# Kernel optimization log

Hardware: AMD Instinct MI355X
Metric: run time of the kernel (lower is better)

## Reference

```python
import math
import jax, jax.numpy as jnp
import numpy as np

D_MODEL = 1024
N_HEADS = 16
HEAD_DIM = 64          # block_size
NUM_RULES = 64
RANK = 8               # proj_rank = round(sqrt(head_dim)); also router_rank
SHARED_RANK = 32       # round(sqrt(d_model))
NUM_BLOCKS = 16        # min(in,out)//block_size = 1024//64; total_block_dim == d_model
B, S = 4, 1024
ROPE_BASE = 10000.0


def setup_inputs() -> dict:
    key = jax.random.key(0)
    ks = iter(jax.random.split(key, 32))
    def nrm(shape, s=0.02):
        return jax.random.normal(next(ks), shape, dtype=jnp.float32) * s
    inp = {
        "x": jax.random.normal(next(ks), (B, S, D_MODEL), dtype=jnp.float32),
        "target_rule_ids": jax.random.randint(next(ks), (B, S), 0, NUM_RULES),
    }
    for p in ("q", "k", "v", "o"):
        inp[p + "_si"] = nrm((D_MODEL, SHARED_RANK))
        inp[p + "_so"] = nrm((SHARED_RANK, D_MODEL))
        inp[p + "_ri"] = nrm((NUM_RULES, HEAD_DIM, RANK))
        inp[p + "_ro"] = nrm((NUM_RULES, RANK, HEAD_DIM))
        inp[p + "_lg"] = nrm((NUM_RULES, NUM_BLOCKS), 1.0 / math.sqrt(NUM_BLOCKS))
    inp["router_q"] = nrm((NUM_RULES, RANK))
    inp["router_k"] = nrm((NUM_RULES, RANK))
    return inp


def _rule_proj(x, rules, si, so, ri, ro, lg):
    """RuleAwareProjection.forward_rules_batched, de-permuted.

    The torch code argsorts tokens by rule, zero-pads per-rule buckets, runs
    bmm per rule and scatters back; mathematically that equals a per-token
    gather of the rule's low-rank adapter, which is what we compute here.
    x: [N, D_MODEL], rules: [N] int.
    """
    base = (x @ si) @ so                                  # shared low-rank path
    xb = x.reshape(-1, NUM_BLOCKS, HEAD_DIM)              # [N, nb, bs]
    h = jnp.einsum('nbs,nsr->nbr', xb, ri[rules])         # [N, nb, rank]
    a = jnp.einsum('nbr,nrt->nbt', h, ro[rules])          # [N, nb, bs]
    # temperature = 1/sqrt(num_blocks) => logits / temperature = logits*sqrt(nb)
    sel = jax.nn.softmax(lg[rules] * math.sqrt(NUM_BLOCKS), axis=-1)
    return base + (a * sel[:, :, None]).reshape(-1, D_MODEL)


def _rope(q, k):
    # q, k: [B, H, S, D]; interleaved-pair rotation, start_pos = 0.
    S_, D = q.shape[2], q.shape[3]
    pos = jnp.arange(S_, dtype=jnp.float32)[:, None]
    div = jnp.exp(jnp.arange(0, D, 2, dtype=jnp.float32) * (-math.log(ROPE_BASE) / D))
    f = pos * div                                         # [S, D/2]
    sin, cos = jnp.sin(f), jnp.cos(f)
    def rot(t):
        t1, t2 = t[..., 0::2], t[..., 1::2]
        return jnp.stack([t1 * cos - t2 * sin, t2 * cos + t1 * sin], axis=-1).reshape(t.shape)
    return rot(q), rot(k)


def reference(x, target_rule_ids,
              q_si, q_so, q_ri, q_ro, q_lg,
              k_si, k_so, k_ri, k_ro, k_lg,
              v_si, v_so, v_ri, v_ro, v_lg,
              o_si, o_so, o_ri, o_ro, o_lg,
              router_q, router_k):
    B_, S_, C = x.shape
    flat_x = x.reshape(-1, C)
    rules = target_rule_ids.reshape(-1)

    q = _rule_proj(flat_x, rules, q_si, q_so, q_ri, q_ro, q_lg)
    k = _rule_proj(flat_x, rules, k_si, k_so, k_ri, k_ro, k_lg)
    v = _rule_proj(flat_x, rules, v_si, v_so, v_ri, v_ro, v_lg)
    q = q.reshape(B_, S_, N_HEADS, HEAD_DIM).transpose(0, 2, 1, 3)
    k = k.reshape(B_, S_, N_HEADS, HEAD_DIM).transpose(0, 2, 1, 3)
    v = v.reshape(B_, S_, N_HEADS, HEAD_DIM).transpose(0, 2, 1, 3)
    q, k = _rope(q, k)

    # rule-routing sparse mask: cosine affinity between token rule embeddings
    rq = router_q[target_rule_ids]                        # [B, S, rank]
    rk = router_k[target_rule_ids]
    rqn = rq / jnp.maximum(jnp.linalg.norm(rq, axis=-1, keepdims=True), 1e-12)
    rkn = rk / jnp.maximum(jnp.linalg.norm(rk, axis=-1, keepdims=True), 1e-12)
    tau = 1.0 / math.log(max(math.e, RANK))
    aff = jnp.einsum('bqr,bkr->bqk', rqn, rkn) / tau       # [B, S, S]
    causal = jnp.tril(jnp.ones((S_, S_), dtype=bool))
    masked = jnp.where(causal[None], aff, -jnp.inf)
    top_k = max(2, int(math.sqrt(S_)))
    if S_ > top_k:
        thr = jax.lax.top_k(masked, top_k)[0][..., -1:]
        rule_mask = (masked >= thr) & causal[None]
    else:
        rule_mask = jnp.broadcast_to(causal[None], masked.shape)

    scores = jnp.einsum('bhqd,bhkd->bhqk', q, k) / math.sqrt(HEAD_DIM)
    scores = jnp.where(rule_mask[:, None], scores, -jnp.inf)
    attn = jax.nn.softmax(scores, axis=-1)
    out = jnp.einsum('bhqk,bhkd->bhqd', attn, v)
    out = out.transpose(0, 2, 1, 3).reshape(-1, C)
    out = _rule_proj(out, rules, o_si, o_so, o_ri, o_ro, o_lg)
    return out.reshape(B_, S_, C)
```

## Files before the change

### kernel.cpp

```cpp
#include <hip/hip_runtime.h>
#include <hip/hip_bf16.h>

#define D_MODEL 1024
#define N_HEADS 16
#define HEAD_DIM 64
#define NUM_RULES 64
#define RANK 8
#define SHARED_RANK 32
#define NUM_BLOCKS_ 16
#define BB 4
#define SS 1024
#define NTOK (BB*SS)
#define NGRP (NTOK/8)
#define NGRP4 (NTOK/4)

typedef __attribute__((ext_vector_type(8))) short bf16x8;
typedef __attribute__((ext_vector_type(4))) float f32x4;

__device__ __forceinline__ float bf2f(unsigned short u) {
  unsigned int i = ((unsigned int)u) << 16;
  float f;
  __builtin_memcpy(&f, &i, 4);
  return f;
}
__device__ __forceinline__ unsigned short f2bf(float f) {
  __hip_bfloat16 h = __float2bfloat16(f);
  unsigned short u;
  __builtin_memcpy(&u, &h, 2);
  return u;
}
__device__ __forceinline__ float u2f(unsigned int i) {
  float f;
  __builtin_memcpy(&f, &i, 4);
  return f;
}
template<bool BF>
__device__ __forceinline__ float ldw(const void* p, size_t i) {
  if (BF) return bf2f(((const unsigned short*)p)[i]);
  else    return ((const float*)p)[i];
}

__device__ __forceinline__ void gload16(const void* g, void* l) {
  __builtin_amdgcn_global_load_lds(
      (const __attribute__((address_space(1))) unsigned int*)g,
      (__attribute__((address_space(3))) unsigned int*)l, 16, 0, 0);
}

__global__ void detect_kernel(const unsigned short* __restrict__ x, int* __restrict__ flag) {
  const int lane = threadIdx.x;
  int good = 0;
  for (int i = 0; i < 4; i++) {
    unsigned short u = x[lane*4 + i];
    int e = (u >> 7) & 0xFF;
    good += (e == 0 || (e >= 100 && e <= 145)) ? 1 : 0;
  }
  for (int off = 32; off; off >>= 1) good += __shfl_xor(good, off);
  if (lane == 0) flag[0] = (good >= 224) ? 1 : 0;
}

template<bool BF>
__device__ __forceinline__ void precompute_body(
    const void* rq, const void* rk,
    const void* qlg, const void* klg, const void* vlg, const void* olg,
    float* __restrict__ M, float* __restrict__ sel)
{
  __shared__ float rqn[64][8], rkn[64][8];
  const int tid = threadIdx.x;
  if (tid < 64) {
    float v[8]; float s = 0.f;
    for (int i = 0; i < 8; i++) { v[i] = ldw<BF>(rq, tid*8+i); s += v[i]*v[i]; }
    float inv = 1.0f / fmaxf(sqrtf(s), 1e-12f);
    for (int i = 0; i < 8; i++) rqn[tid][i] = v[i]*inv;
  } else if (tid < 128) {
    int r = tid - 64;
    float v[8]; float s = 0.f;
    for (int i = 0; i < 8; i++) { v[i] = ldw<BF>(rk, r*8+i); s += v[i]*v[i]; }
    float inv = 1.0f / fmaxf(sqrtf(s), 1e-12f);
    for (int i = 0; i < 8; i++) rkn[r][i] = v[i]*inv;
  }
  __syncthreads();
  const float LN8 = 2.0794415416798357f;
  for (int idx = tid; idx < 64*64; idx += 256) {
    int i = idx >> 6, j = idx & 63;
    float d = 0.f;
    for (int t = 0; t < 8; t++) d += rqn[i][t]*rkn[j][t];
    M[idx] = d * LN8;
  }
  const void* lgs[4] = {qlg, klg, vlg, olg};
  {
    int r = tid & 63;
    const void* lg = lgs[tid >> 6];
    float e[NUM_BLOCKS_]; float mx = -1e30f;
    for (int b = 0; b < NUM_BLOCKS_; b++) {
      e[b] = ldw<BF>(lg, r*NUM_BLOCKS_ + b) * 4.0f;
      mx = fmaxf(mx, e[b]);
    }
    float s = 0.f;
    for (int b = 0; b < NUM_BLOCKS_; b++) { e[b] = expf(e[b]-mx); s += e[b]; }
    float inv = 1.0f/s;
    for (int b = 0; b < NUM_BLOCKS_; b++) sel[tid*NUM_BLOCKS_+b] = e[b]*inv;
  }
}

__global__ void precompute_kernel(
    const void* rq, const void* rk,
    const void* qlg, const void* klg, const void* vlg, const void* olg,
    float* M, float* sel, const int* __restrict__ flag)
{
  if (*flag) precompute_body<true >(rq, rk, qlg, klg, vlg, olg, M, sel);
  else       precompute_body<false>(rq, rk, qlg, klg, vlg, olg, M, sel);
}

__global__ __launch_bounds__(128) void prep_wb_kernel(
    const float* __restrict__ qsi, const float* __restrict__ ksi,
    const float* __restrict__ vsi, const float* __restrict__ osi,
    unsigned short* __restrict__ wh, unsigned short* __restrict__ wl,
    const int* __restrict__ flag)
{
  if (*flag) return;
  const int kt = blockIdx.x, p = blockIdx.y;
  const int tid = threadIdx.x, nt = tid >> 6, lane = tid & 63;
  const float* si = (p==0)?qsi:((p==1)?ksi:((p==2)?vsi:osi));
  const int col = nt*16 + (lane & 15);
  const int k0 = kt*32 + (lane >> 4)*8;
  size_t base = ((((size_t)p*32 + kt)*2 + nt)*64 + lane)*8;
  unsigned short h8[8], l8[8];
  #pragma unroll
  for (int j = 0; j < 8; j++) {
    float f = si[(size_t)(k0 + j)*SHARED_RANK + col];
    unsigned short hu = f2bf(f);
    h8[j] = hu;
    l8[j] = f2bf(f - bf2f(hu));
  }
  #pragma unroll
  for (int j = 0; j < 8; j++) { wh[base + j] = h8[j]; wl[base + j] = l8[j]; }
}

template<int NPROJ>
__device__ __forceinline__ void tt_mfma_body(
    const float* __restrict__ xin,
    const unsigned short* __restrict__ wh, const unsigned short* __restrict__ wl,
    int p0, float* __restrict__ ttg)
{
  const int NT = NPROJ*2;
  const int tile = blockIdx.x;
  const int tid = threadIdx.x, lane = tid & 63, w = tid >> 6;
  const int kq = lane >> 4;
  __shared__ float red[4][64][25];

  f32x4 acc[NT];
  #pragma unroll
  for (int i = 0; i < NT; i++) acc[i] = (f32x4){0.f,0.f,0.f,0.f};

  const float* xrow = xin + (size_t)(tile*16 + (lane & 15))*D_MODEL + kq*8;
  #pragma unroll 2
  for (int s = 0; s < 8; s++) {
    const int kt = w*8 + s;
    float4 a0 = *(const float4*)(xrow + kt*32);
    float4 a1 = *(const float4*)(xrow + kt*32 + 4);
    float av[8] = {a0.x,a0.y,a0.z,a0.w,a1.x,a1.y,a1.z,a1.w};
    bf16x8 ah, al;
    #pragma unroll
    for (int j = 0; j < 8; j++) {
      unsigned short hu = f2bf(av[j]);
      ah[j] = (short)hu;
      al[j] = (short)f2bf(av[j] - bf2f(hu));
    }
    #pragma unroll
    for (int p = 0; p < NPROJ; p++) {
      #pragma unroll
      for (int nt = 0; nt < 2; nt++) {
        size_t bidx = ((((size_t)(p0+p)*32 + kt)*2 + nt)*64 + lane)*8;
        bf16x8 bh = *(const bf16x8*)(wh + bidx);
        bf16x8 bl = *(const bf16x8*)(wl + bidx);
        f32x4 c = acc[p*2+nt];
        c = __builtin_amdgcn_mfma_f32_16x16x32_bf16(ah, bh, c, 0, 0, 0);
        c = __builtin_amdgcn_mfma_f32_16x16x32_bf16(al, bh, c, 0, 0, 0);
        c = __builtin_amdgcn_mfma_f32_16x16x32_bf16(ah, bl, c, 0, 0, 0);
        acc[p*2+nt] = c;
      }
    }
  }
  #pragma unroll
  for (int i = 0; i < NT; i++) {
    red[w][lane][i*4+0] = acc[i][0]; red[w][lane][i*4+1] = acc[i][1];
    red[w][lane][i*4+2] = acc[i][2]; red[w][lane][i*4+3] = acc[i][3];
  }
  __syncthreads();
  if (w == 0) {
    const int tok0 = tile*16 + (lane >> 4)*4;
    #pragma unroll
    for (int i = 0; i < NT; i++) {
      const int ys = i >> 1, jj = (i & 1)*16 + (lane & 15);
      #pragma unroll
      for (int r = 0; r < 4; r++) {
        float sum = red[0][lane][i*4+r] + red[1][lane][i*4+r]
                  + red[2][lane][i*4+r] + red[3][lane][i*4+r];
        ttg[((size_t)ys*NTOK + tok0 + r)*32 + jj] = sum;
      }
    }
  }
}

__global__ __launch_bounds__(256) void A_tt_mfma3(
    const float* __restrict__ xin,
    const unsigned short* __restrict__ wh, const unsigned short* __restrict__ wl,
    float* __restrict__ ttg, const int* __restrict__ flag)
{
  if (*flag) return;
  tt_mfma_body<3>(xin, wh, wl, 0, ttg);
}

__global__ __launch_bounds__(256) void A_tt_mfma1(
    const float* __restrict__ xin,
    const unsigned short* __restrict__ wh, const unsigned short* __restrict__ wl,
    float* __restrict__ ttg, const int* __restrict__ flag)
{
  if (*flag) return;
  tt_mfma_body<1>(xin, wh, wl, 3, ttg);
}

template<int NP>
__device__ __forceinline__ void hh_body(
    const float* __restrict__ xin, const int* __restrict__ rules,
    const float* __restrict__ ri0, const float* __restrict__ ri1,
    const float* __restrict__ ri2, float* __restrict__ hhg)
{
  const int g = blockIdx.x, n0 = g*8, tid = threadIdx.x;
  const int t = tid >> 5, blk = (tid >> 1) & 15, r0 = (tid & 1)*4;
  const int n = n0 + t;
  const int rule = rules[n];
  const float* xb = xin + (size_t)n*D_MODEL + blk*64;
  const float* wb[3];
  wb[0] = ri0 + (size_t)rule*512 + r0;
  if (NP > 1) {
    wb[1] = ri1 + (size_t)rule*512 + r0;
    wb[2] = ri2 + (size_t)rule*512 + r0;
  }
  float a[NP][4];
  #pragma unroll
  for (int p = 0; p < NP; p++) { a[p][0]=0.f; a[p][1]=0.f; a[p][2]=0.f; a[p][3]=0.f; }
  #pragma unroll 4
  for (int k4 = 0; k4 < 16; k4++) {
    float4 xv = *(const float4*)(xb + k4*4);
    #pragma unroll
    for (int q = 0; q < 4; q++) {
      const int k = k4*4 + q;
      float xq = (q==0)?xv.x:((q==1)?xv.y:((q==2)?xv.z:xv.w));
      #pragma unroll
      for (int p = 0; p < NP; p++) {
        float4 wv = *(const float4*)(wb[p] + (size_t)k*8);
        a[p][0] += xq*wv.x; a[p][1] += xq*wv.y; a[p][2] += xq*wv.z; a[p][3] += xq*wv.w;
      }
    }
  }
  #pragma unroll
  for (int p = 0; p < NP; p++) {
    float4 hv; hv.x=a[p][0]; hv.y=a[p][1]; hv.z=a[p][2]; hv.w=a[p][3];
    *(float4*)&hhg[((size_t)p*NTOK + n)*128 + blk*8 + r0] = hv;
  }
}

__global__ __launch_bounds__(256) void A_hh3_f32(
    const float* __restrict__ xin, const int* __restrict__ rules,
    const float* __restrict__ qri, const float* __restrict__ kri,
    const float* __restrict__ vri, float* __restrict__ hhg,
    const int* __restrict__ flag)
{
  if (*flag) return;
  hh_body<3>(xin, rules, qri, kri, vri, hhg);
}

__global__ __launch_bounds__(256) void A_hh1_f32(
    const float* __restrict__ xin, const int* __restrict__ rules,
    const float* __restrict__ ori, float* __restrict__ hhg,
    const int* __restrict__ flag)
{
  if (*flag) return;
  hh_body<1>(xin, rules, ori, ori, ori, hhg);
}

template<bool IN_BF, bool W_BF>
__device__ __forceinline__ void stageA_body(
    const void* __restrict__ xin, const int* __restrict__ rules,
    const void* __restrict__ si, const void* __restrict__ ri,
    float* __restrict__ ttg, float* __restrict__ hhg, int yslot)
{
  const int g = blockIdx.x, n0 = g*8, tid = threadIdx.x;
  __shared__ float xs[8][D_MODEL];
  __shared__ float tpart[8][32][9];
  __shared__ int rl[8];

  #pragma unroll
  for (int t = 0; t < 8; t++) {
    float4 f;
    if (IN_BF) {
      ushort4 u = ((const ushort4*)((const unsigned short*)xin + (size_t)(n0+t)*D_MODEL))[tid];
      f.x = bf2f(u.x); f.y = bf2f(u.y); f.z = bf2f(u.z); f.w = bf2f(u.w);
    } else {
      f = ((const float4*)xin)[(size_t)(n0+t)*(D_MODEL/4) + tid];
    }
    *(float4*)&xs[t][tid*4] = f;
  }
  if (tid < 8) rl[tid] = rules[n0 + tid];
  __syncthreads();

  {
    const int c = tid >> 5, j = tid & 31;
    float p[8];
    #pragma unroll
    for (int t = 0; t < 8; t++) p[t] = 0.f;
    #pragma unroll 4
    for (int d4 = 0; d4 < 32; d4++) {
      const int d = c*128 + d4*4;
      float w0 = ldw<W_BF>(si, (size_t)(d+0)*SHARED_RANK + j);
      float w1 = ldw<W_BF>(si, (size_t)(d+1)*SHARED_RANK + j);
      float w2 = ldw<W_BF>(si, (size_t)(d+2)*SHARED_RANK + j);
      float w3 = ldw<W_BF>(si, (size_t)(d+3)*SHARED_RANK + j);
      #pragma unroll
      for (int t = 0; t < 8; t++) {
        float4 xv = *(const float4*)&xs[t][d];
        p[t] += xv.x*w0 + xv.y*w1 + xv.z*w2 + xv.w*w3;
      }
    }
    #pragma unroll
    for (int t = 0; t < 8; t++) tpart[c][j][t] = p[t];
  }
  __syncthreads();

  {
    const int t = tid >> 5, j = tid & 31;
    float s = 0.f;
    #pragma unroll
    for (int c = 0; c < 8; c++) s += tpart[c][j][t];
    ttg[((size_t)yslot*NTOK + n0 + t)*32 + j] = s;
  }
  {
    const int t = tid >> 5, blk = (tid >> 1) & 15, r0 = (tid & 1)*4;
    const int rule = rl[t];
    float a0=0.f, a1=0.f, a2=0.f, a3=0.f;
    #pragma unroll 4
    for (int k4 = 0; k4 < 16; k4++) {
      const int kk = ((k4 + blk) & 15) * 4;
      float4 xv = *(const float4*)&xs[t][blk*64 + kk];
      #pragma unroll
      for (int q = 0; q < 4; q++) {
        const int k = kk + q;
        float w0,w1,w2,w3;
        if (W_BF) {
          ushort4 u = *(const ushort4*)((const unsigned short*)ri + (size_t)rule*512 + (size_t)k*8 + r0);
          w0=bf2f(u.x); w1=bf2f(u.y); w2=bf2f(u.z); w3=bf2f(u.w);
        } else {
          float4 u = *(const float4*)((const float*)ri + (size_t)rule*512 + (size_t)k*8 + r0);
          w0=u.x; w1=u.y; w2=u.z; w3=u.w;
        }
        float xq = (q==0)?xv.x:((q==1)?xv.y:((q==2)?xv.z:xv.w));
        a0 += xq*w0; a1 += xq*w1; a2 += xq*w2; a3 += xq*w3;
      }
    }
    float4 hv; hv.x=a0; hv.y=a1; hv.z=a2; hv.w=a3;
    *(float4*)&hhg[((size_t)yslot*NTOK + n0 + t)*128 + blk*8 + r0] = hv;
  }
}

__global__ __launch_bounds__(256) void A_qkv_bf16(
    const void* x, const int* rules,
    const void* qsi, const void* qri, const void* ksi, const void* kri,
    const void* vsi, const void* vri,
    float* ttg, float* hhg, const int* __restrict__ flag)
{
  if (!*flag) return;
  const int y = blockIdx.y;
  const void* si = (y==0)?qsi:((y==1)?ksi:vsi);
  const void* ri = (y==0)?qri:((y==1)?kri:vri);
  stageA_body<true,true>(x, rules, si, ri, ttg, hhg, y);
}

__global__ __launch_bounds__(256) void A_o_bf16(
    const void* ain, const int* rules, const void* osi, const void* ori,
    float* ttg, float* hhg, const int* __restrict__ flag)
{
  if (!*flag) return;
  stageA_body<false,true>(ain, rules, osi, ori, ttg, hhg, 0);
}

template<bool W_BF>
__device__ __forceinline__ void stageB_body(
    const float* __restrict__ ttg, const float* __restrict__ hhg,
    const int* __restrict__ rules,
    const void* __restrict__ so, const void* __restrict__ ro,
    const float* __restrict__ sel, void* __restrict__ out,
    int yslot, int do_rope, int out_bf)
{
  const int blk4 = blockIdx.x;
  const int n0 = blk4*4, tid = threadIdx.x;
  __shared__ float tt_lds[32][5];
  __shared__ float hh_lds[4][132];
  __shared__ int rl[4];

  if (tid < 128) {
    const int j = tid >> 2, t4 = tid & 3;
    tt_lds[j][t4] = ttg[((size_t)yslot*NTOK + n0 + t4)*32 + j];
  } else if (tid < 256 && (tid - 128) < 128) {
    const int i = tid - 128;
    const int t4 = i >> 5, c = (i*4) & 127;
    float4 hv = *(const float4*)&hhg[((size_t)yslot*NTOK + n0 + t4)*128 + c];
    *(float4*)&hh_lds[t4][c] = hv;
  }
  if (tid < 4) rl[tid] = rules[n0 + tid];
  __syncthreads();

  const int ch0 = tid*4;
  float a0[4], a1[4], a2[4], a3[4];
  #pragma unroll
  for (int t = 0; t < 4; t++) { a0[t]=0.f; a1[t]=0.f; a2[t]=0.f; a3[t]=0.f; }

  #pragma unroll 4
  for (int j = 0; j < 32; j++) {
    float w0, w1, w2, w3;
    if (W_BF) {
      ushort4 u = *(const ushort4*)((const unsigned short*)so + (size_t)j*D_MODEL + ch0);
      w0=bf2f(u.x); w1=bf2f(u.y); w2=bf2f(u.z); w3=bf2f(u.w);
    } else {
      float4 u = *(const float4*)((const float*)so + (size_t)j*D_MODEL + ch0);
      w0=u.x; w1=u.y; w2=u.z; w3=u.w;
    }
    #pragma unroll
    for (int t = 0; t < 4; t++) {
      float tv = tt_lds[j][t];
      a0[t] += tv*w0; a1[t] += tv*w1; a2[t] += tv*w2; a3[t] += tv*w3;
    }
  }

  const int blk = ch0 >> 6, tc = ch0 & 63;
  float inv0 = 0.f, inv1 = 0.f;
  if (do_rope) {
    inv0 = expf(-(float)tc     * (9.210340371976184f/64.0f));
    inv1 = expf(-(float)(tc+2) * (9.210340371976184f/64.0f));
  }
  #pragma unroll 2
  for (int t = 0; t < 4; t++) {
    const int rule = rl[t];
    float b0=0.f, b1=0.f, b2=0.f, b3=0.f;
    #pragma unroll
    for (int r = 0; r < 8; r++) {
      float w0,w1,w2,w3;
      if (W_BF) {
        ushort4 u = *(const ushort4*)((const unsigned short*)ro + (size_t)rule*512 + r*64 + tc);
        w0=bf2f(u.x); w1=bf2f(u.y); w2=bf2f(u.z); w3=bf2f(u.w);
      } else {
        float4 u = *(const float4*)((const float*)ro + (size_t)rule*512 + r*64 + tc);
        w0=u.x; w1=u.y; w2=u.z; w3=u.w;
      }
      float hv = hh_lds[t][blk*8 + r];
      b0 += hv*w0; b1 += hv*w1; b2 += hv*w2; b3 += hv*w3;
    }
    float sb = sel[rule*NUM_BLOCKS_ + blk];
    float e0 = a0[t] + b0*sb, o0 = a1[t] + b1*sb;
    float e1 = a2[t] + b2*sb, o1 = a3[t] + b3*sb;
    const int n = n0 + t;
    if (do_rope) {
      float spos = (float)(n & (SS-1));
      float sn0, cs0, sn1, cs1;
      sincosf(spos*inv0, &sn0, &cs0);
      sincosf(spos*inv1, &sn1, &cs1);
      float u0 = e0*cs0 - o0*sn0; o0 = o0*cs0 + e0*sn0; e0 = u0;
      float u1 = e1*cs1 - o1*sn1; o1 = o1*cs1 + e1*sn1; e1 = u1;
    }
    if (out_bf) {
      ushort4 uv; uv.x=f2bf(e0); uv.y=f2bf(o0); uv.z=f2bf(e1); uv.w=f2bf(o1);
      *(ushort4*)((unsigned short*)out + (size_t)n*D_MODEL + ch0) = uv;
    } else {
      float4 fv; fv.x=e0; fv.y=o0; fv.z=e1; fv.w=o1;
      *(float4*)((float*)out + (size_t)n*D_MODEL + ch0) = fv;
    }
  }
}

__global__ __launch_bounds__(256) void B_qkv_bf16(
    const float* ttg, const float* hhg, const int* rules,
    const void* qso, const void* qro, const void* kso, const void* kro,
    const void* vso, const void* vro,
    const float* sel, float* qb, unsigned short* kb, unsigned short* vb,
    const int* __restrict__ flag)
{
  if (!*flag) return;
  const int y = blockIdx.y;
  const void* so = (y==0)?qso:((y==1)?kso:vso);
  const void* ro = (y==0)?qro:((y==1)?kro:vro);
  void* out = (y==0)?(void*)qb:((y==1)?(void*)kb:(void*)vb);
  stageB_body<true>(ttg, hhg, rules, so, ro, sel + y*1024, out, y, (y<2)?1:0, (y>=1)?1:0);
}

__global__ __launch_bounds__(256) void B_qkv_f32(
    const float* ttg, const float* hhg, const int* rules,
    const void* qso, const void* qro, const void* kso, const void* kro,
    const void* vso, const void* vro,
    const float* sel, float* qb, unsigned short* kb, unsigned short* vb,
    const int* __restrict__ flag)
{
  if (*flag) return;
  const int y = blockIdx.y;
  const void* so = (y==0)?qso:((y==1)?kso:vso);
  const void* ro = (y==0)?qro:((y==1)?kro:vro);
  void* out = (y==0)?(void*)qb:((y==1)?(void*)kb:(void*)vb);
  stageB_body<false>(ttg, hhg, rules, so, ro, sel + y*1024, out, y, (y<2)?1:0, (y>=1)?1:0);
}

__global__ __launch_bounds__(256) void B_o_bf16(
    const float* ttg, const float* hhg, const int* rules,
    const void* oso, const void* oro, const float* sel, void* out,
    const int* __restrict__ flag)
{
  if (!*flag) return;
  stageB_body<true>(ttg, hhg, rules, oso, oro, sel, out, 0, 0, 1);
}

__global__ __launch_bounds__(256) void B_o_f32(
    const float* ttg, const float* hhg, const int* rules,
    const void* oso, const void* oro, const float* sel, void* out,
    const int* __restrict__ flag)
{
  if (*flag) return;
  stageB_body<false>(ttg, hhg, rules, oso, oro, sel, out, 0, 0, 0);
}

__global__ __launch_bounds__(64) void mask_kernel(
    const int* __restrict__ rules, const float* __restrict__ M,
    unsigned long long* __restrict__ am)
{
  const int bid = blockIdx.x;
  const int b = bid >> 10, qi = bid & 1023;
  const int lane = threadIdx.x;
  __shared__ int rrow[SS];
  __shared__ float val[64];
  __shared__ int cnth[64];
  for (int i = lane; i < SS/4; i += 64)
    ((int4*)rrow)[i] = ((const int4*)(rules + b*SS))[i];
  cnth[lane] = 0;
  __syncthreads();
  for (int k = lane; k <= qi; k += 64) atomicAdd(&cnth[rrow[k]], 1);
  const int qrule = rrow[qi];
  const float myv = M[qrule*64 + lane];
  val[lane] = myv;
  __syncthreads();
  const int c = cnth[lane];
  int A = 0;
  for (int r = 0; r < 64; r++) {
    int cr = __shfl(c, r);
    A += (val[r] > myv) ? cr : 0;
  }
  unsigned long long allowed = __ballot(A < 32);
  if (lane == 0) am[bid] = allowed;
}

__global__ __launch_bounds__(256) void vtrans_kernel(
    const unsigned short* __restrict__ vb, unsigned short* __restrict__ vt)
{
  const int st = blockIdx.x, h = blockIdx.y, b = blockIdx.z;
  __shared__ unsigned short t[64][72];
  const int tid = threadIdx.x;
  #pragma unroll
  for (int it = 0; it < 2; it++) {
    int i = tid + it*256;
    int r = i >> 3, c8 = (i & 7)*8;
    uint4 v = *(const uint4*)(vb + ((size_t)(b*SS + st*64 + r)*D_MODEL + h*HEAD_DIM + c8));
    t[c8+0][r] = (unsigned short)(v.x & 0xffffu);
    t[c8+1][r] = (unsigned short)(v.x >> 16);
    t[c8+2][r] = (unsigned short)(v.y & 0xffffu);
    t[c8+3][r] = (unsigned short)(v.y >> 16);
    t[c8+4][r] = (unsigned short)(v.z & 0xffffu);
    t[c8+5][r] = (unsigned short)(v.z >> 16);
    t[c8+6][r] = (unsigned short)(v.w & 0xffffu);
    t[c8+7][r] = (unsigned short)(v.w >> 16);
  }
  __syncthreads();
  #pragma unroll
  for (int it = 0; it < 2; it++) {
    int i = tid + it*256;
    int d = i >> 3, c8 = i & 7;
    uint4 o = *(const uint4*)&t[d][c8*8];
    *(uint4*)(vt + ((size_t)(b*N_HEADS + h)*HEAD_DIM + d)*SS + st*64 + c8*8) = o;
  }
}

__global__ __launch_bounds__(256) void attn_mfma_kernel(
    const float* __restrict__ qb,
    const unsigned short* __restrict__ kb,
    const unsigned short* __restrict__ vtb,
    const int* __restrict__ rules,
    const unsigned long long* __restrict__ am,
    float* outb)
{
  const int qx = blockIdx.x, b = blockIdx.y, h = blockIdx.z;
  const int tid = threadIdx.x, lane = tid & 63, w = tid >> 6;
  __shared__ unsigned short Ks[2][64*64];
  __shared__ unsigned short Vs[2][64*64];
  __shared__ unsigned short Pl[4][16*64];
  __shared__ int rl[SS];

  ((int4*)rl)[tid] = ((const int4*)(rules + b*SS))[tid];

  const unsigned short* kbase = kb + (size_t)b*SS*D_MODEL + h*HEAD_DIM;
  const unsigned short* vbase = vtb + (size_t)(b*N_HEADS + h)*HEAD_DIM*SS;

  const int srow0 = tid >> 3;
  const int spos  = tid & 7;
  unsigned short* pw = &Pl[w][0];

  for (int halfq = 0; halfq < 2; halfq++) {
    const int qt = halfq ? (15 - qx) : qx;

    const int qa = qt*64 + w*16 + (lane & 15);
    bf16x8 qfrag[2];
    {
      const float* qrow = qb + (size_t)(b*SS + qa)*D_MODEL + h*HEAD_DIM + (lane>>4)*8;
      #pragma unroll
      for (int kc = 0; kc < 2; kc++) {
        float4 f0 = *(const float4*)(qrow + kc*32);
        float4 f1 = *(const float4*)(qrow + kc*32 + 4);
        bf16x8 qv;
        qv[0] = (short)f2bf(f0.x*0.125f); qv[1] = (short)f2bf(f0.y*0.125f);
        qv[2] = (short)f2bf(f0.z*0.125f); qv[3] = (short)f2bf(f0.w*0.125f);
        qv[4] = (short)f2bf(f1.x*0.125f); qv[5] = (short)f2bf(f1.y*0.125f);
        qv[6] = (short)f2bf(f1.z*0.125f); qv[7] = (short)f2bf(f1.w*0.125f);
        qfrag[kc] = qv;
      }
    }
    int qg[4]; unsigned aqlo[4], aqhi[4];
    #pragma unroll
    for (int r = 0; r < 4; r++) {
      qg[r] = qt*64 + w*16 + (lane>>4)*4 + r;
      uint2 mm = *(const uint2*)(am + (size_t)b*SS + qg[r]);
      aqlo[r] = mm.x; aqhi[r] = mm.y;
    }
    f32x4 Oacc[4];
    #pragma unroll
    for (int nt = 0; nt < 4; nt++) Oacc[nt] = (f32x4){0.f,0.f,0.f,0.f};
    float mrun[4], lrun[4];
    #pragma unroll
    for (int r = 0; r < 4; r++) { mrun[r] = -1e30f; lrun[r] = 0.f; }

    #pragma unroll
    for (int it = 0; it < 2; it++) {
      int row = srow0 + it*32;
      int sc = spos ^ (row & 7);
      gload16(kbase + (size_t)row*D_MODEL + sc*8, &Ks[0][(row*8 + spos)*8]);
      gload16(vbase + (size_t)row*SS + sc*8,      &Vs[0][(row*8 + spos)*8]);
    }
    __syncthreads();

    int cur = 0;
    for (int kt = 0; kt <= qt; kt++) {
      if (kt < qt) {
        const size_t koff = (size_t)(kt + 1)*64;
        #pragma unroll
        for (int it = 0; it < 2; it++) {
          int row = srow0 + it*32;
          int sc = spos ^ (row & 7);
          gload16(kbase + (koff + row)*D_MODEL + sc*8, &Ks[cur^1][(row*8 + spos)*8]);
          gload16(vbase + (size_t)row*SS + koff + sc*8, &Vs[cur^1][(row*8 + spos)*8]);
        }
      }
      const unsigned short* kt_lds = Ks[cur];
      const unsigned short* vt_lds = Vs[cur];

      f32x4 Sacc[4];
      #pragma unroll
      for (int nt = 0; nt < 4; nt++) {
        const int key = nt*16 + (lane & 15);
        f32x4 c = (f32x4){0.f,0.f,0.f,0.f};
        #pragma unroll
        for (int kc = 0; kc < 2; kc++) {
          int off = (key*128 + kc*64 + (lane>>4)*16) ^ ((key & 7) << 4);
          bf16x8 kf = *(const bf16x8*)((const char*)kt_lds + off);
          c = __builtin_amdgcn_mfma_f32_16x16x32_bf16(qfrag[kc], kf, c, 0, 0, 0);
        }
        Sacc[nt] = c;
      }

      float sv[4][4];
      #pragma unroll
      for (int nt = 0; nt < 4; nt++) {
        const int k = kt*64 + nt*16 + (lane & 15);
        const int rr = rl[k];
        const unsigned sh = (unsigned)rr & 31u;
        const bool hi = rr >= 32;
        #pragma unroll
        for (int r = 0; r < 4; r++) {
          unsigned bits = hi ? aqhi[r] : aqlo[r];
          bool ok = (((bits >> sh) & 1u) != 0u) && (k <= qg[r]);
          sv[nt][r] = ok ? Sacc[nt][r] : -3e38f;
        }
      }

      float tm[4];
      #pragma unroll
      for (int r = 0; r < 4; r++)
        tm[r] = fmaxf(fmaxf(sv[0][r], sv[1][r]), fmaxf(sv[2][r], sv[3][r]));
      #pragma unroll
      for (int off = 1; off < 16; off <<= 1) {
        #pragma unroll
        for (int r = 0; r < 4; r++) tm[r] = fmaxf(tm[r], __shfl_xor(tm[r], off));
      }
      float alpha[4];
      #pragma unroll
      for (int r = 0; r < 4; r++) {
        float nm = fmaxf(mrun[r], tm[r]);
        alpha[r] = __expf(mrun[r] - nm);
        mrun[r] = nm;
      }
      float ps[4] = {0.f, 0.f, 0.f, 0.f};
      #pragma unroll
      for (int nt = 0; nt < 4; nt++) {
        #pragma unroll
        for (int r = 0; r < 4; r++) {
          float p = __expf(sv[nt][r] - mrun[r]);
          ps[r] += p;
          const int q = (lane>>4)*4 + r;
          int off = (q*128 + (nt*16 + (lane & 15))*2) ^ ((q & 7) << 4);
          *(unsigned short*)((char*)pw + off) = f2bf(p);
        }
      }
      #pragma unroll
      for (int off = 1; off < 16; off <<= 1) {
        #pragma unroll
        for (int r = 0; r < 4; r++) ps[r] += __shfl_xor(ps[r], off);
      }
      #pragma unroll
      for (int r = 0; r < 4; r++) lrun[r] = lrun[r]*alpha[r] + ps[r];
      #pragma unroll
      for (int nt = 0; nt < 4; nt++) {
        Oacc[nt][0] *= alpha[0]; Oacc[nt][1] *= alpha[1];
        Oacc[nt][2] *= alpha[2]; Oacc[nt][3] *= alpha[3];
      }

      #pragma unroll
      for (int kc = 0; kc < 2; kc++) {
        const int qrow = lane & 15;
        int aoff = (qrow*128 + kc*64 + (lane>>4)*16) ^ ((qrow & 7) << 4);
        bf16x8 pa = *(const bf16x8*)((const char*)pw + aoff);
        #pragma unroll
        for (int nt = 0; nt < 4; nt++) {
          const int d = nt*16 + (lane & 15);
          int boff = (d*128 + kc*64 + (lane>>4)*16) ^ ((d & 7) << 4);
          bf16x8 vf = *(const bf16x8*)((const char*)vt_lds + boff);
          Oacc[nt] = __builtin_amdgcn_mfma_f32_16x16x32_bf16(pa, vf, Oacc[nt], 0, 0, 0);
        }
      }
      __syncthreads();
      cur ^= 1;
    }

    float invl[4];
    #pragma unroll
    for (int r = 0; r < 4; r++) invl[r] = 1.0f / lrun[r];
    #pragma unroll
    for (int nt = 0; nt < 4; nt++) {
      #pragma unroll
      for (int r = 0; r < 4; r++) {
        outb[(size_t)(b*SS + qg[r])*D_MODEL + h*HEAD_DIM + nt*16 + (lane & 15)]
            = Oacc[nt][r]*invl[r];
      }
    }
  }
}

extern "C" void kernel_launch(void* const* d_in, const int* in_sizes, int n_in,
                              void* d_out, int out_size, void* d_ws, size_t ws_size,
                              hipStream_t stream) {
  (void)in_sizes; (void)n_in; (void)out_size; (void)ws_size;
  const void* x    = d_in[0];
  const int* rules = (const int*)d_in[1];
  const void* q_si = d_in[2];  const void* q_so = d_in[3];
  const void* q_ri = d_in[4];  const void* q_ro = d_in[5];  const void* q_lg = d_in[6];
  const void* k_si = d_in[7];  const void* k_so = d_in[8];
  const void* k_ri = d_in[9];  const void* k_ro = d_in[10]; const void* k_lg = d_in[11];
  const void* v_si = d_in[12]; const void* v_so = d_in[13];
  const void* v_ri = d_in[14]; const void* v_ro = d_in[15]; const void* v_lg = d_in[16];
  const void* o_si = d_in[17]; const void* o_so = d_in[18];
  const void* o_ri = d_in[19]; const void* o_ro = d_in[20]; const void* o_lg = d_in[21];
  const void* rq   = d_in[22]; const void* rk   = d_in[23];

  char* ws = (char*)d_ws;
  const size_t MB = 1024*1024;
  float*          qb    = (float*)(ws);
  unsigned short* kb    = (unsigned short*)(ws + 16*MB);
  unsigned short* vb    = (unsigned short*)(ws + 24*MB);
  unsigned short* vtb   = (unsigned short*)(ws + 32*MB);
  float*          ttg   = (float*)(ws + 40*MB);
  float*          hhg   = (float*)(ws + 42*MB);
  unsigned long long* amask = (unsigned long long*)(ws + 48*MB);
  float*          Mt    = (float*)(ws + 49*MB + 16*1024);
  float*          selt  = (float*)(ws + 49*MB + 32*1024);
  int*            flag  = (int*)  (ws + 49*MB + 48*1024);
  unsigned short* wpkh  = (unsigned short*)(ws + 49*MB + 64*1024);
  unsigned short* wpkl  = (unsigned short*)(ws + 49*MB + 64*1024 + 256*1024);

  detect_kernel<<<1, 64, 0, stream>>>((const unsigned short*)x, flag);
  precompute_kernel<<<1, 256, 0, stream>>>(rq, rk, q_lg, k_lg, v_lg, o_lg, Mt, selt, flag);
  mask_kernel<<<NTOK, 64, 0, stream>>>(rules, Mt, amask);
  prep_wb_kernel<<<dim3(32, 4), 128, 0, stream>>>(
      (const float*)q_si, (const float*)k_si, (const float*)v_si, (const float*)o_si,
      wpkh, wpkl, flag);

  A_qkv_bf16<<<dim3(NGRP, 3), 256, 0, stream>>>(x, rules, q_si, q_ri, k_si, k_ri, v_si, v_ri, ttg, hhg, flag);
  A_tt_mfma3<<<256, 256, 0, stream>>>((const float*)x, wpkh, wpkl, ttg, flag);
  A_hh3_f32<<<NGRP, 256, 0, stream>>>((const float*)x, rules,
      (const float*)q_ri, (const float*)k_ri, (const float*)v_ri, hhg, flag);

  B_qkv_bf16<<<dim3(NGRP4, 3), 256, 0, stream>>>(ttg, hhg, rules, q_so, q_ro, k_so, k_ro, v_so, v_ro,
                                                 selt, qb, kb, vb, flag);
  B_qkv_f32 <<<dim3(NGRP4, 3), 256, 0, stream>>>(ttg, hhg, rules, q_so, q_ro, k_so, k_ro, v_so, v_ro,
                                                 selt, qb, kb, vb, flag);

  vtrans_kernel<<<dim3(16, 16, 4), 256, 0, stream>>>(vb, vtb);
  attn_mfma_kernel<<<dim3(8, BB, N_HEADS), 256, 0, stream>>>(qb, kb, vtb, rules, amask, qb);

  A_o_bf16<<<dim3(NGRP, 1), 256, 0, stream>>>(qb, rules, o_si, o_ri, ttg, hhg, flag);
  A_tt_mfma1<<<256, 256, 0, stream>>>(qb, wpkh, wpkl, ttg, flag);
  A_hh1_f32<<<NGRP, 256, 0, stream>>>(qb, rules, (const float*)o_ri, hhg, flag);
  B_o_bf16<<<NGRP4, 256, 0, stream>>>(ttg, hhg, rules, o_so, o_ro, selt + 3*1024, d_out, flag);
  B_o_f32 <<<NGRP4, 256, 0, stream>>>(ttg, hhg, rules, o_so, o_ro, selt + 3*1024, d_out, flag);
}
```

Baseline: 275.5 us.

## Split attention into one q-tile per block, pack key rules, merge B kernels

The attention kernel now launches 16 blocks along x, each handling one query tile with a reordered mapping, instead of 8 blocks each looping over a paired short and long tile. This gives more blocks for occupancy and adds a launch bound of 4 blocks per SM. The per-key rule lookups move from an LDS-staged rules array to a byte-packed rule table built in mask_kernel and read per key tile. The bf16 and f32 B-stage kernels are merged into single kernels that branch on the flag, which removes the empty launches. Without the tile pairing the per-block work is uneven, so the scheduler has to balance the load.

```diff
diff --git a/kernel.cpp b/kernel.cpp
--- a/kernel.cpp
+++ b/kernel.cpp
@@ -477,57 +477,35 @@
   }
 }
 
-__global__ __launch_bounds__(256) void B_qkv_bf16(
+__global__ __launch_bounds__(256) void B_qkv(
     const float* ttg, const float* hhg, const int* rules,
     const void* qso, const void* qro, const void* kso, const void* kro,
     const void* vso, const void* vro,
     const float* sel, float* qb, unsigned short* kb, unsigned short* vb,
     const int* __restrict__ flag)
 {
-  if (!*flag) return;
   const int y = blockIdx.y;
   const void* so = (y==0)?qso:((y==1)?kso:vso);
   const void* ro = (y==0)?qro:((y==1)?kro:vro);
   void* out = (y==0)?(void*)qb:((y==1)?(void*)kb:(void*)vb);
-  stageB_body<true>(ttg, hhg, rules, so, ro, sel + y*1024, out, y, (y<2)?1:0, (y>=1)?1:0);
-}
-
-__global__ __launch_bounds__(256) void B_qkv_f32(
-    const float* ttg, const float* hhg, const int* rules,
-    const void* qso, const void* qro, const void* kso, const void* kro,
-    const void* vso, const void* vro,
-    const float* sel, float* qb, unsigned short* kb, unsigned short* vb,
-    const int* __restrict__ flag)
-{
-  if (*flag) return;
-  const int y = blockIdx.y;
-  const void* so = (y==0)?qso:((y==1)?kso:vso);
-  const void* ro = (y==0)?qro:((y==1)?kro:vro);
-  void* out = (y==0)?(void*)qb:((y==1)?(void*)kb:(void*)vb);
-  stageB_body<false>(ttg, hhg, rules, so, ro, sel + y*1024, out, y, (y<2)?1:0, (y>=1)?1:0);
-}
-
-__global__ __launch_bounds__(256) void B_o_bf16(
+  if (*flag)
+    stageB_body<true >(ttg, hhg, rules, so, ro, sel + y*1024, out, y, (y<2)?1:0, (y>=1)?1:0);
+  else
+    stageB_body<false>(ttg, hhg, rules, so, ro, sel + y*1024, out, y, (y<2)?1:0, (y>=1)?1:0);
+}
+
+__global__ __launch_bounds__(256) void B_o(
     const float* ttg, const float* hhg, const int* rules,
     const void* oso, const void* oro, const float* sel, void* out,
     const int* __restrict__ flag)
 {
-  if (!*flag) return;
-  stageB_body<true>(ttg, hhg, rules, oso, oro, sel, out, 0, 0, 1);
-}
-
-__global__ __launch_bounds__(256) void B_o_f32(
-    const float* ttg, const float* hhg, const int* rules,
-    const void* oso, const void* oro, const float* sel, void* out,
-    const int* __restrict__ flag)
-{
-  if (*flag) return;
-  stageB_body<false>(ttg, hhg, rules, oso, oro, sel, out, 0, 0, 0);
+  if (*flag) stageB_body<true >(ttg, hhg, rules, oso, oro, sel, out, 0, 0, 1);
+  else       stageB_body<false>(ttg, hhg, rules, oso, oro, sel, out, 0, 0, 0);
 }
 
 __global__ __launch_bounds__(64) void mask_kernel(
     const int* __restrict__ rules, const float* __restrict__ M,
-    unsigned long long* __restrict__ am)
+    unsigned long long* __restrict__ am, unsigned int* __restrict__ rp)
 {
   const int bid = blockIdx.x;
   const int b = bid >> 10, qi = bid & 1023;
@@ -539,6 +517,13 @@
     ((int4*)rrow)[i] = ((const int4*)(rules + b*SS))[i];
   cnth[lane] = 0;
   __syncthreads();
+  if (qi < 16 && lane < 16) {
+    unsigned v = 0;
+    #pragma unroll
+    for (int nt = 0; nt < 4; nt++)
+      v |= ((unsigned)rrow[qi*64 + nt*16 + lane] & 0xffu) << (8*nt);
+    rp[b*256 + qi*16 + lane] = v;
+  }
   for (int k = lane; k <= qi; k += 64) atomicAdd(&cnth[rrow[k]], 1);
   const int qrule = rrow[qi];
   const float myv = M[qrule*64 + lane];
@@ -584,184 +569,180 @@
   }
 }
 
-__global__ __launch_bounds__(256) void attn_mfma_kernel(
+__global__ __launch_bounds__(256, 4) void attn_mfma_kernel(
     const float* __restrict__ qb,
     const unsigned short* __restrict__ kb,
     const unsigned short* __restrict__ vtb,
-    const int* __restrict__ rules,
+    const unsigned int* __restrict__ rp,
     const unsigned long long* __restrict__ am,
     float* outb)
 {
-  const int qx = blockIdx.x, b = blockIdx.y, h = blockIdx.z;
+  const int x = blockIdx.x, b = blockIdx.y, h = blockIdx.z;
+  const int qt = (x < 8) ? x : (23 - x);
   const int tid = threadIdx.x, lane = tid & 63, w = tid >> 6;
   __shared__ unsigned short Ks[2][64*64];
   __shared__ unsigned short Vs[2][64*64];
   __shared__ unsigned short Pl[4][16*64];
-  __shared__ int rl[SS];
-
-  ((int4*)rl)[tid] = ((const int4*)(rules + b*SS))[tid];
 
   const unsigned short* kbase = kb + (size_t)b*SS*D_MODEL + h*HEAD_DIM;
   const unsigned short* vbase = vtb + (size_t)(b*N_HEADS + h)*HEAD_DIM*SS;
+  const unsigned int* rpb = rp + b*256;
 
   const int srow0 = tid >> 3;
   const int spos  = tid & 7;
   unsigned short* pw = &Pl[w][0];
 
-  for (int halfq = 0; halfq < 2; halfq++) {
-    const int qt = halfq ? (15 - qx) : qx;
-
-    const int qa = qt*64 + w*16 + (lane & 15);
-    bf16x8 qfrag[2];
-    {
-      const float* qrow = qb + (size_t)(b*SS + qa)*D_MODEL + h*HEAD_DIM + (lane>>4)*8;
+  const int qa = qt*64 + w*16 + (lane & 15);
+  bf16x8 qfrag[2];
+  {
+    const float* qrow = qb + (size_t)(b*SS + qa)*D_MODEL + h*HEAD_DIM + (lane>>4)*8;
+    #pragma unroll
+    for (int kc = 0; kc < 2; kc++) {
+      float4 f0 = *(const float4*)(qrow + kc*32);
+      float4 f1 = *(const float4*)(qrow + kc*32 + 4);
+      bf16x8 qv;
+      qv[0] = (short)f2bf(f0.x*0.125f); qv[1] = (short)f2bf(f0.y*0.125f);
+      qv[2] = (short)f2bf(f0.z*0.125f); qv[3] = (short)f2bf(f0.w*0.125f);
+      qv[4] = (short)f2bf(f1.x*0.125f); qv[5] = (short)f2bf(f1.y*0.125f);
+      qv[6] = (short)f2bf(f1.z*0.125f); qv[7] = (short)f2bf(f1.w*0.125f);
+      qfrag[kc] = qv;
+    }
+  }
+  int qg[4]; unsigned aqlo[4], aqhi[4];
+  #pragma unroll
+  for (int r = 0; r < 4; r++) {
+    qg[r] = qt*64 + w*16 + (lane>>4)*4 + r;
+    uint2 mm = *(const uint2*)(am + (size_t)b*SS + qg[r]);
+    aqlo[r] = mm.x; aqhi[r] = mm.y;
+  }
+  f32x4 Oacc[4];
+  #pragma unroll
+  for (int nt = 0; nt < 4; nt++) Oacc[nt] = (f32x4){0.f,0.f,0.f,0.f};
+  float mrun[4], lrun[4];
+  #pragma unroll
+  for (int r = 0; r < 4; r++) { mrun[r] = -1e30f; lrun[r] = 0.f; }
+
+  #pragma unroll
+  for (int it = 0; it < 2; it++) {
+    int row = srow0 + it*32;
+    int sc = spos ^ (row & 7);
+    gload16(kbase + (size_t)row*D_MODEL + sc*8, &Ks[0][(row*8 + spos)*8]);
+    gload16(vbase + (size_t)row*SS + sc*8,      &Vs[0][(row*8 + spos)*8]);
+  }
+  __syncthreads();
+
+  int cur = 0;
+  for (int kt = 0; kt <= qt; kt++) {
+    const unsigned ru = rpb[kt*16 + (lane & 15)];
+    if (kt < qt) {
+      const size_t koff = (size_t)(kt + 1)*64;
+      #pragma unroll
+      for (int it = 0; it < 2; it++) {
+        int row = srow0 + it*32;
+        int sc = spos ^ (row & 7);
+        gload16(kbase + (koff + row)*D_MODEL + sc*8, &Ks[cur^1][(row*8 + spos)*8]);
+        gload16(vbase + (size_t)row*SS + koff + sc*8, &Vs[cur^1][(row*8 + spos)*8]);
+      }
+    }
+    const unsigned short* kt_lds = Ks[cur];
+    const unsigned short* vt_lds = Vs[cur];
+
+    f32x4 Sacc[4];
+    #pragma unroll
+    for (int nt = 0; nt < 4; nt++) {
+      const int key = nt*16 + (lane & 15);
+      f32x4 c = (f32x4){0.f,0.f,0.f,0.f};
       #pragma unroll
       for (int kc = 0; kc < 2; kc++) {
-        float4 f0 = *(const float4*)(qrow + kc*32);
-        float4 f1 = *(const float4*)(qrow + kc*32 + 4);
-        bf16x8 qv;
-        qv[0] = (short)f2bf(f0.x*0.125f); qv[1] = (short)f2bf(f0.y*0.125f);
-        qv[2] = (short)f2bf(f0.z*0.125f); qv[3] = (short)f2bf(f0.w*0.125f);
-        qv[4] = (short)f2bf(f1.x*0.125f); qv[5] = (short)f2bf(f1.y*0.125f);
-        qv[6] = (short)f2bf(f1.z*0.125f); qv[7] = (short)f2bf(f1.w*0.125f);
-        qfrag[kc] = qv;
-      }
-    }
-    int qg[4]; unsigned aqlo[4], aqhi[4];
+        int off = (key*128 + kc*64 + (lane>>4)*16) ^ ((key & 7) << 4);
+        bf16x8 kf = *(const bf16x8*)((const char*)kt_lds + off);
+        c = __builtin_amdgcn_mfma_f32_16x16x32_bf16(qfrag[kc], kf, c, 0, 0, 0);
+      }
+      Sacc[nt] = c;
+    }
+
+    float sv[4][4];
+    #pragma unroll
+    for (int nt = 0; nt < 4; nt++) {
+      const int k = kt*64 + nt*16 + (lane & 15);
+      const unsigned rr = (ru >> (nt*8)) & 0xffu;
+      const unsigned sh = rr & 31u;
+      const bool hi = rr >= 32;
+      #pragma unroll
+      for (int r = 0; r < 4; r++) {
+        unsigned bits = hi ? aqhi[r] : aqlo[r];
+        bool ok = (((bits >> sh) & 1u) != 0u) && (k <= qg[r]);
+        sv[nt][r] = ok ? Sacc[nt][r] : -3e38f;
+      }
+    }
+
+    float tm[4];
+    #pragma unroll
+    for (int r = 0; r < 4; r++)
+      tm[r] = fmaxf(fmaxf(sv[0][r], sv[1][r]), fmaxf(sv[2][r], sv[3][r]));
+    #pragma unroll
+    for (int off = 1; off < 16; off <<= 1) {
+      #pragma unroll
+      for (int r = 0; r < 4; r++) tm[r] = fmaxf(tm[r], __shfl_xor(tm[r], off));
+    }
+    float alpha[4];
     #pragma unroll
     for (int r = 0; r < 4; r++) {
-      qg[r] = qt*64 + w*16 + (lane>>4)*4 + r;
-      uint2 mm = *(const uint2*)(am + (size_t)b*SS + qg[r]);
-      aqlo[r] = mm.x; aqhi[r] = mm.y;
-    }
-    f32x4 Oacc[4];
-    #pragma unroll
-    for (int nt = 0; nt < 4; nt++) Oacc[nt] = (f32x4){0.f,0.f,0.f,0.f};
-    float mrun[4], lrun[4];
-    #pragma unroll
-    for (int r = 0; r < 4; r++) { mrun[r] = -1e30f; lrun[r] = 0.f; }
-
-    #pragma unroll
-    for (int it = 0; it < 2; it++) {
-      int row = srow0 + it*32;
-      int sc = spos ^ (row & 7);
-      gload16(kbase + (size_t)row*D_MODEL + sc*8, &Ks[0][(row*8 + spos)*8]);
-      gload16(vbase + (size_t)row*SS + sc*8,      &Vs[0][(row*8 + spos)*8]);
+      float nm = fmaxf(mrun[r], tm[r]);
+      alpha[r] = __expf(mrun[r] - nm);
+      mrun[r] = nm;
+    }
+    float ps[4] = {0.f, 0.f, 0.f, 0.f};
+    #pragma unroll
+    for (int nt = 0; nt < 4; nt++) {
+      #pragma unroll
+      for (int r = 0; r < 4; r++) {
+        float p = __expf(sv[nt][r] - mrun[r]);
+        ps[r] += p;
+        const int q = (lane>>4)*4 + r;
+        int off = (q*128 + (nt*16 + (lane & 15))*2) ^ ((q & 7) << 4);
+        *(unsigned short*)((char*)pw + off) = f2bf(p);
+      }
+    }
+    #pragma unroll
+    for (int off = 1; off < 16; off <<= 1) {
+      #pragma unroll
+      for (int r = 0; r < 4; r++) ps[r] += __shfl_xor(ps[r], off);
+    }
+    #pragma unroll
+    for (int r = 0; r < 4; r++) lrun[r] = lrun[r]*alpha[r] + ps[r];
+    #pragma unroll
+    for (int nt = 0; nt < 4; nt++) {
+      Oacc[nt][0] *= alpha[0]; Oacc[nt][1] *= alpha[1];
+      Oacc[nt][2] *= alpha[2]; Oacc[nt][3] *= alpha[3];
+    }
+
+    #pragma unroll
+    for (int kc = 0; kc < 2; kc++) {
+      const int qrow = lane & 15;
+      int aoff = (qrow*128 + kc*64 + (lane>>4)*16) ^ ((qrow & 7) << 4);
+      bf16x8 pa = *(const bf16x8*)((const char*)pw + aoff);
+      #pragma unroll
+      for (int nt = 0; nt < 4; nt++) {
+        const int d = nt*16 + (lane & 15);
+        int boff = (d*128 + kc*64 + (lane>>4)*16) ^ ((d & 7) << 4);
+        bf16x8 vf = *(const bf16x8*)((const char*)vt_lds + boff);
+        Oacc[nt] = __builtin_amdgcn_mfma_f32_16x16x32_bf16(pa, vf, Oacc[nt], 0, 0, 0);
+      }
     }
     __syncthreads();
-
-    int cur = 0;
-    for (int kt = 0; kt <= qt; kt++) {
-      if (kt < qt) {
-        const size_t koff = (size_t)(kt + 1)*64;
-        #pragma unroll
-        for (int it = 0; it < 2; it++) {
-          int row = srow0 + it*32;
-          int sc = spos ^ (row & 7);
-          gload16(kbase + (koff + row)*D_MODEL + sc*8, &Ks[cur^1][(row*8 + spos)*8]);
-          gload16(vbase + (size_t)row*SS + koff + sc*8, &Vs[cur^1][(row*8 + spos)*8]);
-        }
-      }
-      const unsigned short* kt_lds = Ks[cur];
-      const unsigned short* vt_lds = Vs[cur];
-
-      f32x4 Sacc[4];
-      #pragma unroll
-      for (int nt = 0; nt < 4; nt++) {
-        const int key = nt*16 + (lane & 15);
-        f32x4 c = (f32x4){0.f,0.f,0.f,0.f};
-        #pragma unroll
-        for (int kc = 0; kc < 2; kc++) {
-          int off = (key*128 + kc*64 + (lane>>4)*16) ^ ((key & 7) << 4);
-          bf16x8 kf = *(const bf16x8*)((const char*)kt_lds + off);
-          c = __builtin_amdgcn_mfma_f32_16x16x32_bf16(qfrag[kc], kf, c, 0, 0, 0);
-        }
-        Sacc[nt] = c;
-      }
-
-      float sv[4][4];
-      #pragma unroll
-      for (int nt = 0; nt < 4; nt++) {
-        const int k = kt*64 + nt*16 + (lane & 15);
-        const int rr = rl[k];
-        const unsigned sh = (unsigned)rr & 31u;
-        const bool hi = rr >= 32;
-        #pragma unroll
-        for (int r = 0; r < 4; r++) {
-          unsigned bits = hi ? aqhi[r] : aqlo[r];
-          bool ok = (((bits >> sh) & 1u) != 0u) && (k <= qg[r]);
-          sv[nt][r] = ok ? Sacc[nt][r] : -3e38f;
-        }
-      }
-
-      float tm[4];
-      #pragma unroll
-      for (int r = 0; r < 4; r++)
-        tm[r] = fmaxf(fmaxf(sv[0][r], sv[1][r]), fmaxf(sv[2][r], sv[3][r]));
-      #pragma unroll
-      for (int off = 1; off < 16; off <<= 1) {
-        #pragma unroll
-        for (int r = 0; r < 4; r++) tm[r] = fmaxf(tm[r], __shfl_xor(tm[r], off));
-      }
-      float alpha[4];
-      #pragma unroll
-      for (int r = 0; r < 4; r++) {
-        float nm = fmaxf(mrun[r], tm[r]);
-        alpha[r] = __expf(mrun[r] - nm);
-        mrun[r] = nm;
-      }
-      float ps[4] = {0.f, 0.f, 0.f, 0.f};
-      #pragma unroll
-      for (int nt = 0; nt < 4; nt++) {
-        #pragma unroll
-        for (int r = 0; r < 4; r++) {
-          float p = __expf(sv[nt][r] - mrun[r]);
-          ps[r] += p;
-          const int q = (lane>>4)*4 + r;
-          int off = (q*128 + (nt*16 + (lane & 15))*2) ^ ((q & 7) << 4);
-          *(unsigned short*)((char*)pw + off) = f2bf(p);
-        }
-      }
-      #pragma unroll
-      for (int off = 1; off < 16; off <<= 1) {
-        #pragma unroll
-        for (int r = 0; r < 4; r++) ps[r] += __shfl_xor(ps[r], off);
-      }
-      #pragma unroll
-      for (int r = 0; r < 4; r++) lrun[r] = lrun[r]*alpha[r] + ps[r];
-      #pragma unroll
-      for (int nt = 0; nt < 4; nt++) {
-        Oacc[nt][0] *= alpha[0]; Oacc[nt][1] *= alpha[1];
-        Oacc[nt][2] *= alpha[2]; Oacc[nt][3] *= alpha[3];
-      }
-
-      #pragma unroll
-      for (int kc = 0; kc < 2; kc++) {
-        const int qrow = lane & 15;
-        int aoff = (qrow*128 + kc*64 + (lane>>4)*16) ^ ((qrow & 7) << 4);
-        bf16x8 pa = *(const bf16x8*)((const char*)pw + aoff);
-        #pragma unroll
-        for (int nt = 0; nt < 4; nt++) {
-          const int d = nt*16 + (lane & 15);
-          int boff = (d*128 + kc*64 + (lane>>4)*16) ^ ((d & 7) << 4);
-          bf16x8 vf = *(const bf16x8*)((const char*)vt_lds + boff);
-          Oacc[nt] = __builtin_amdgcn_mfma_f32_16x16x32_bf16(pa, vf, Oacc[nt], 0, 0, 0);
-        }
-      }
-      __syncthreads();
-      cur ^= 1;
-    }
-
-    float invl[4];
-    #pragma unroll
-    for (int r = 0; r < 4; r++) invl[r] = 1.0f / lrun[r];
-    #pragma unroll
-    for (int nt = 0; nt < 4; nt++) {
-      #pragma unroll
-      for (int r = 0; r < 4; r++) {
-        outb[(size_t)(b*SS + qg[r])*D_MODEL + h*HEAD_DIM + nt*16 + (lane & 15)]
-            = Oacc[nt][r]*invl[r];
-      }
+    cur ^= 1;
+  }
+
+  float invl[4];
+  #pragma unroll
+  for (int r = 0; r < 4; r++) invl[r] = 1.0f / lrun[r];
+  #pragma unroll
+  for (int nt = 0; nt < 4; nt++) {
+    #pragma unroll
+    for (int r = 0; r < 4; r++) {
+      outb[(size_t)(b*SS + qg[r])*D_MODEL + h*HEAD_DIM + nt*16 + (lane & 15)]
+          = Oacc[nt][r]*invl[r];
     }
   }
 }
@@ -794,12 +775,13 @@
   float*          Mt    = (float*)(ws + 49*MB + 16*1024);
   float*          selt  = (float*)(ws + 49*MB + 32*1024);
   int*            flag  = (int*)  (ws + 49*MB + 48*1024);
+  unsigned int*   rp    = (unsigned int*)(ws + 49*MB + 52*1024);
   unsigned short* wpkh  = (unsigned short*)(ws + 49*MB + 64*1024);
   unsigned short* wpkl  = (unsigned short*)(ws + 49*MB + 64*1024 + 256*1024);
 
   detect_kernel<<<1, 64, 0, stream>>>((const unsigned short*)x, flag);
   precompute_kernel<<<1, 256, 0, stream>>>(rq, rk, q_lg, k_lg, v_lg, o_lg, Mt, selt, flag);
-  mask_kernel<<<NTOK, 64, 0, stream>>>(rules, Mt, amask);
+  mask_kernel<<<NTOK, 64, 0, stream>>>(rules, Mt, amask, rp);
   prep_wb_kernel<<<dim3(32, 4), 128, 0, stream>>>(
       (const float*)q_si, (const float*)k_si, (const float*)v_si, (const float*)o_si,
       wpkh, wpkl, flag);
@@ -809,17 +791,14 @@
   A_hh3_f32<<<NGRP, 256, 0, stream>>>((const float*)x, rules,
       (const float*)q_ri, (const float*)k_ri, (const float*)v_ri, hhg, flag);
 
-  B_qkv_bf16<<<dim3(NGRP4, 3), 256, 0, stream>>>(ttg, hhg, rules, q_so, q_ro, k_so, k_ro, v_so, v_ro,
-                                                 selt, qb, kb, vb, flag);
-  B_qkv_f32 <<<dim3(NGRP4, 3), 256, 0, stream>>>(ttg, hhg, rules, q_so, q_ro, k_so, k_ro, v_so, v_ro,
-                                                 selt, qb, kb, vb, flag);
+  B_qkv<<<dim3(NGRP4, 3), 256, 0, stream>>>(ttg, hhg, rules, q_so, q_ro, k_so, k_ro, v_so, v_ro,
+                                            selt, qb, kb, vb, flag);
 
   vtrans_kernel<<<dim3(16, 16, 4), 256, 0, stream>>>(vb, vtb);
-  attn_mfma_kernel<<<dim3(8, BB, N_HEADS), 256, 0, stream>>>(qb, kb, vtb, rules, amask, qb);
+  attn_mfma_kernel<<<dim3(16, BB, N_HEADS), 256, 0, stream>>>(qb, kb, vtb, rp, amask, qb);
 
   A_o_bf16<<<dim3(NGRP, 1), 256, 0, stream>>>(qb, rules, o_si, o_ri, ttg, hhg, flag);
   A_tt_mfma1<<<256, 256, 0, stream>>>(qb, wpkh, wpkl, ttg, flag);
   A_hh1_f32<<<NGRP, 256, 0, stream>>>(qb, rules, (const float*)o_ri, hhg, flag);
-  B_o_bf16<<<NGRP4, 256, 0, stream>>>(ttg, hhg, rules, o_so, o_ro, selt + 3*1024, d_out, flag);
-  B_o_f32 <<<NGRP4, 256, 0, stream>>>(ttg, hhg, rules, o_so, o_ro, selt + 3*1024, d_out, flag);
-}
+  B_o<<<NGRP4, 256, 0, stream>>>(ttg, hhg, rules, o_so, o_ro, selt + 3*1024, d_out, flag);
+}
```

Result: slower. 284.3 us (+3.2%).
